# Kernel optimization log

Hardware: AMD Instinct MI355X
Metric: run time of the kernel (lower is better)

Reference implementation:

```python
import jax, jax.numpy as jnp
import numpy as np

EPS = 1e-05
N = 1_000_000
D = 128
G = 4096


def setup_inputs() -> dict:
    key = jax.random.key(0)
    k1, k2 = jax.random.split(key)
    features = jax.random.normal(k1, (N, D), dtype=jnp.float32)
    segment_ids = jnp.sort(jax.random.randint(k2, (N,), 0, G, dtype=jnp.int32))
    return {
        "features": features,
        "segment_ids": segment_ids,
        "num_graphs": G,
        "weight": jnp.ones((D,), jnp.float32),
        "bias": jnp.zeros((D,), jnp.float32),
        "mean_scale": jnp.ones((D,), jnp.float32),
    }


def reference(features, segment_ids, num_graphs, weight, bias, mean_scale):
    # per-graph node counts (clamped to 1 to avoid 0/0 for empty segments)
    counts = jax.ops.segment_sum(jnp.ones((features.shape[0],), features.dtype),
                                 segment_ids, num_segments=num_graphs)
    counts = jnp.maximum(counts, 1.0)[:, None]  # [G, 1]
    # segment mean
    mean = jax.ops.segment_sum(features, segment_ids, num_segments=num_graphs) / counts
    out = features - mean[segment_ids] * mean_scale  # [N, D]
    # segment variance of shifted features
    var = jax.ops.segment_sum(out * out, segment_ids, num_segments=num_graphs) / counts
    std = jnp.sqrt(var + EPS)  # [G, D]
    return weight * out / std[segment_ids] + bias
```

## Files before the change

### kernel.cpp

```cpp
#include <hip/hip_runtime.h>

#define DIM   128
#define DIM4  32
#define NGRAPH 4096
#define EPSV  1e-5f

__global__ __launch_bounds__(256) void gn_stats(
    const float* __restrict__ feat, const int* __restrict__ seg,
    const float* __restrict__ weight, const float* __restrict__ bias,
    const float* __restrict__ mscale,
    float* __restrict__ A, float* __restrict__ B, int N)
{
    const int g = blockIdx.x;

    int lo = 0, hi = N;
    while (lo < hi) { int mid = (lo + hi) >> 1; if (seg[mid] < g) lo = mid + 1; else hi = mid; }
    const int start = lo;
    hi = N;
    while (lo < hi) { int mid = (lo + hi) >> 1; if (seg[mid] < g + 1) lo = mid + 1; else hi = mid; }
    const int end = lo;

    const int tid  = threadIdx.x;
    const int dim4 = tid & 31;
    const int noff = tid >> 5;

    float4 s = make_float4(0.f, 0.f, 0.f, 0.f);
    float4 q = make_float4(0.f, 0.f, 0.f, 0.f);
    for (int n = start + noff; n < end; n += 8) {
        const float4 x = ((const float4*)(feat + (size_t)n * DIM))[dim4];
        s.x += x.x; s.y += x.y; s.z += x.z; s.w += x.w;
        q.x += x.x * x.x; q.y += x.y * x.y; q.z += x.z * x.z; q.w += x.w * x.w;
    }

    __shared__ float4 ls[256];
    __shared__ float4 lq[256];
    ls[tid] = s; lq[tid] = q;
    __syncthreads();
    for (int off = 128; off >= 32; off >>= 1) {
        if (tid < off) {
            float4 a = ls[tid], b = ls[tid + off];
            a.x += b.x; a.y += b.y; a.z += b.z; a.w += b.w; ls[tid] = a;
            float4 c = lq[tid], d = lq[tid + off];
            c.x += d.x; c.y += d.y; c.z += d.z; c.w += d.w; lq[tid] = c;
        }
        __syncthreads();
    }

    if (tid < 32) {
        const int   cnt   = (end - start) > 1 ? (end - start) : 1;
        const float inv_c = 1.0f / (float)cnt;
        const float4 S = ls[tid];
        const float4 Q = lq[tid];
#pragma unroll
        for (int j = 0; j < 4; ++j) {
            const int   d   = tid * 4 + j;
            const float Sv  = (&S.x)[j];
            const float Qv  = (&Q.x)[j];
            const float m   = Sv * inv_c;
            const float sc  = mscale[d];
            const float var = Qv * inv_c - m * m * sc * (2.0f - sc);
            const float inv = rsqrtf(var + EPSV);
            const float a   = weight[d] * inv;
            const float b   = bias[d] - m * sc * a;
            A[(size_t)g * DIM + d] = a;
            B[(size_t)g * DIM + d] = b;
        }
    }
}

__global__ __launch_bounds__(256) void gn_apply_g(
    const float* __restrict__ feat, const int* __restrict__ seg,
    const float* __restrict__ A, const float* __restrict__ B,
    float* __restrict__ out, int N)
{
    const int g = blockIdx.x;

    int lo = 0, hi = N;
    while (lo < hi) { int mid = (lo + hi) >> 1; if (seg[mid] < g) lo = mid + 1; else hi = mid; }
    const int start = lo;
    hi = N;
    while (lo < hi) { int mid = (lo + hi) >> 1; if (seg[mid] < g + 1) lo = mid + 1; else hi = mid; }
    const int end = lo;
    if (start >= end) return;

    const int tid  = threadIdx.x;
    const int dim4 = tid & 31;
    const int noff = tid >> 5;

    const float4 a = ((const float4*)A)[(size_t)g * DIM4 + dim4];
    const float4 b = ((const float4*)B)[(size_t)g * DIM4 + dim4];

    for (int n = start + noff; n < end; n += 8) {
        const float4 x = ((const float4*)(feat + (size_t)n * DIM))[dim4];
        float4 r;
        r.x = fmaf(x.x, a.x, b.x);
        r.y = fmaf(x.y, a.y, b.y);
        r.z = fmaf(x.z, a.z, b.z);
        r.w = fmaf(x.w, a.w, b.w);
        ((float4*)(out + (size_t)n * DIM))[dim4] = r;
    }
}

extern "C" void kernel_launch(void* const* d_in, const int* in_sizes, int n_in,
                              void* d_out, int out_size, void* d_ws, size_t ws_size,
                              hipStream_t stream) {
    const float* feat   = (const float*)d_in[0];
    const int*   seg    = (const int*)d_in[1];
    const float* weight = (const float*)d_in[3];
    const float* bias   = (const float*)d_in[4];
    const float* mscale = (const float*)d_in[5];
    float*       out    = (float*)d_out;
    const int N = in_sizes[1];

    float* A = (float*)d_ws;
    float* B = A + (size_t)NGRAPH * DIM;

    hipLaunchKernelGGL(gn_stats, dim3(NGRAPH), dim3(256), 0, stream,
                       feat, seg, weight, bias, mscale, A, B, N);

    hipLaunchKernelGGL(gn_apply_g, dim3(NGRAPH), dim3(256), 0, stream,
                       feat, seg, A, B, out, N);
}
```

Baseline: 1.023 ms.

## Fuse stats and apply passes with precomputed segment offsets and LDS staging

Adds a small kernel that builds the segment offset table once, replacing the two binary searches that every block did in both kernels. Merges the statistics and normalize kernels into one per-graph kernel. The first rows of each segment (up to 92) are kept in LDS so the apply phase does not reread them from memory. Also replaces the shared-memory tree reduction with a shuffle plus cross-wave reduction, and uses nontemporal loads and stores for the rest. The large LDS buffer (about 47KB per block) limits occupancy, and the rows beyond the staged ones still have to be read a second time.

```diff
diff --git a/kernel.cpp b/kernel.cpp
--- a/kernel.cpp
+++ b/kernel.cpp
@@ -1,56 +1,77 @@
 #include <hip/hip_runtime.h>
 
-#define DIM   128
-#define DIM4  32
+#define DIM    128
+#define DIM4   32
 #define NGRAPH 4096
-#define EPSV  1e-5f
+#define EPSV   1e-5f
+#define STAGE_N 92
 
-__global__ __launch_bounds__(256) void gn_stats(
-    const float* __restrict__ feat, const int* __restrict__ seg,
+typedef float f32x4 __attribute__((ext_vector_type(4)));
+
+__global__ __launch_bounds__(256) void seg_offsets(
+    const int* __restrict__ seg, int* __restrict__ off, int N)
+{
+    const int i = blockIdx.x * 256 + threadIdx.x;
+    if (i >= N) return;
+    const int s    = seg[i];
+    const int prev = (i == 0) ? -1 : seg[i - 1];
+    for (int g = prev + 1; g <= s; ++g) off[g] = i;
+    if (i == N - 1) {
+        for (int g = s + 1; g <= NGRAPH; ++g) off[g] = N;
+    }
+}
+
+__global__ __launch_bounds__(256) void gn_fused(
+    const float* __restrict__ feat, const int* __restrict__ off,
     const float* __restrict__ weight, const float* __restrict__ bias,
-    const float* __restrict__ mscale,
-    float* __restrict__ A, float* __restrict__ B, int N)
+    const float* __restrict__ mscale, float* __restrict__ out)
 {
-    const int g = blockIdx.x;
-
-    int lo = 0, hi = N;
-    while (lo < hi) { int mid = (lo + hi) >> 1; if (seg[mid] < g) lo = mid + 1; else hi = mid; }
-    const int start = lo;
-    hi = N;
-    while (lo < hi) { int mid = (lo + hi) >> 1; if (seg[mid] < g + 1) lo = mid + 1; else hi = mid; }
-    const int end = lo;
+    const int g     = blockIdx.x;
+    const int start = off[g];
+    const int end   = off[g + 1];
+    const int cnt   = end - start;
+    if (cnt <= 0) return;
 
     const int tid  = threadIdx.x;
     const int dim4 = tid & 31;
     const int noff = tid >> 5;
+    const int wave = tid >> 6;
+    const int lane = tid & 63;
+
+    __shared__ float4 stage[STAGE_N * DIM4];
+    __shared__ float4 red_s[4][32];
+    __shared__ float4 red_q[4][32];
+    __shared__ float4 Ash[32];
+    __shared__ float4 Bsh[32];
 
     float4 s = make_float4(0.f, 0.f, 0.f, 0.f);
     float4 q = make_float4(0.f, 0.f, 0.f, 0.f);
-    for (int n = start + noff; n < end; n += 8) {
-        const float4 x = ((const float4*)(feat + (size_t)n * DIM))[dim4];
+    for (int i = noff; i < cnt; i += 8) {
+        const float4 x = ((const float4*)(feat + (size_t)(start + i) * DIM))[dim4];
         s.x += x.x; s.y += x.y; s.z += x.z; s.w += x.w;
         q.x += x.x * x.x; q.y += x.y * x.y; q.z += x.z * x.z; q.w += x.w * x.w;
+        if (i < STAGE_N) stage[i * DIM4 + dim4] = x;
     }
 
-    __shared__ float4 ls[256];
-    __shared__ float4 lq[256];
-    ls[tid] = s; lq[tid] = q;
+    s.x += __shfl_down(s.x, 32); s.y += __shfl_down(s.y, 32);
+    s.z += __shfl_down(s.z, 32); s.w += __shfl_down(s.w, 32);
+    q.x += __shfl_down(q.x, 32); q.y += __shfl_down(q.y, 32);
+    q.z += __shfl_down(q.z, 32); q.w += __shfl_down(q.w, 32);
+    if (lane < 32) { red_s[wave][lane] = s; red_q[wave][lane] = q; }
     __syncthreads();
-    for (int off = 128; off >= 32; off >>= 1) {
-        if (tid < off) {
-            float4 a = ls[tid], b = ls[tid + off];
-            a.x += b.x; a.y += b.y; a.z += b.z; a.w += b.w; ls[tid] = a;
-            float4 c = lq[tid], d = lq[tid + off];
-            c.x += d.x; c.y += d.y; c.z += d.z; c.w += d.w; lq[tid] = c;
-        }
-        __syncthreads();
-    }
 
     if (tid < 32) {
-        const int   cnt   = (end - start) > 1 ? (end - start) : 1;
+        float4 S = red_s[0][tid];
+        float4 Q = red_q[0][tid];
+#pragma unroll
+        for (int w = 1; w < 4; ++w) {
+            const float4 a = red_s[w][tid];
+            S.x += a.x; S.y += a.y; S.z += a.z; S.w += a.w;
+            const float4 c = red_q[w][tid];
+            Q.x += c.x; Q.y += c.y; Q.z += c.z; Q.w += c.w;
+        }
         const float inv_c = 1.0f / (float)cnt;
-        const float4 S = ls[tid];
-        const float4 Q = lq[tid];
+        float4 av, bv;
 #pragma unroll
         for (int j = 0; j < 4; ++j) {
             const int   d   = tid * 4 + j;
@@ -62,42 +83,33 @@
             const float inv = rsqrtf(var + EPSV);
             const float a   = weight[d] * inv;
             const float b   = bias[d] - m * sc * a;
-            A[(size_t)g * DIM + d] = a;
-            B[(size_t)g * DIM + d] = b;
+            (&av.x)[j] = a;
+            (&bv.x)[j] = b;
         }
+        Ash[tid] = av; Bsh[tid] = bv;
     }
-}
+    __syncthreads();
 
-__global__ __launch_bounds__(256) void gn_apply_g(
-    const float* __restrict__ feat, const int* __restrict__ seg,
-    const float* __restrict__ A, const float* __restrict__ B,
-    float* __restrict__ out, int N)
-{
-    const int g = blockIdx.x;
+    const float4 a  = Ash[dim4];
+    const float4 b  = Bsh[dim4];
+    const int    sm = cnt < STAGE_N ? cnt : STAGE_N;
 
-    int lo = 0, hi = N;
-    while (lo < hi) { int mid = (lo + hi) >> 1; if (seg[mid] < g) lo = mid + 1; else hi = mid; }
-    const int start = lo;
-    hi = N;
-    while (lo < hi) { int mid = (lo + hi) >> 1; if (seg[mid] < g + 1) lo = mid + 1; else hi = mid; }
-    const int end = lo;
-    if (start >= end) return;
-
-    const int tid  = threadIdx.x;
-    const int dim4 = tid & 31;
-    const int noff = tid >> 5;
-
-    const float4 a = ((const float4*)A)[(size_t)g * DIM4 + dim4];
-    const float4 b = ((const float4*)B)[(size_t)g * DIM4 + dim4];
-
-    for (int n = start + noff; n < end; n += 8) {
-        const float4 x = ((const float4*)(feat + (size_t)n * DIM))[dim4];
-        float4 r;
+    for (int i = noff; i < cnt; i += 8) {
+        float4 x;
+        if (i < sm) {
+            x = stage[i * DIM4 + dim4];
+        } else {
+            const f32x4* p = (const f32x4*)(feat + (size_t)(start + i) * DIM) + dim4;
+            const f32x4 xv = __builtin_nontemporal_load(p);
+            x.x = xv.x; x.y = xv.y; x.z = xv.z; x.w = xv.w;
+        }
+        f32x4 r;
         r.x = fmaf(x.x, a.x, b.x);
         r.y = fmaf(x.y, a.y, b.y);
         r.z = fmaf(x.z, a.z, b.z);
         r.w = fmaf(x.w, a.w, b.w);
-        ((float4*)(out + (size_t)n * DIM))[dim4] = r;
+        f32x4* po = (f32x4*)(out + (size_t)(start + i) * DIM) + dim4;
+        __builtin_nontemporal_store(r, po);
     }
 }
 
@@ -112,12 +124,11 @@
     float*       out    = (float*)d_out;
     const int N = in_sizes[1];
 
-    float* A = (float*)d_ws;
-    float* B = A + (size_t)NGRAPH * DIM;
+    int* off = (int*)d_ws;
 
-    hipLaunchKernelGGL(gn_stats, dim3(NGRAPH), dim3(256), 0, stream,
-                       feat, seg, weight, bias, mscale, A, B, N);
-
-    hipLaunchKernelGGL(gn_apply_g, dim3(NGRAPH), dim3(256), 0, stream,
-                       feat, seg, A, B, out, N);
+    const int blocks0 = (N + 255) / 256;
+    hipLaunchKernelGGL(seg_offsets, dim3(blocks0), dim3(256), 0, stream,
+                       seg, off, N);
+    hipLaunchKernelGGL(gn_fused, dim3(NGRAPH), dim3(256), 0, stream,
+                       feat, off, weight, bias, mscale, out);
 }
```

New measurement: 875.7 us. 14.4% less time.
